# Optimization experiments

Measured on AMD Instinct MI355X. Metric: run time of the kernel, lower is better.

## Reference

```python
import jax, jax.numpy as jnp
import numpy as np

N_WIRES = 8
DIM = 2 ** N_WIRES  # 256 amplitudes
# PauliZ sign table: Z_SIGNS[w, i] = +1 if bit w of basis index i is 0 else -1
_bits = (np.arange(DIM)[None, :] >> (N_WIRES - 1 - np.arange(N_WIRES))[:, None]) & 1
Z_SIGNS = jnp.asarray(1.0 - 2.0 * _bits, dtype=jnp.float32)  # [8, 256]


def quantum_project(t, theta):
    """Batched 8-wire circuit: RX(x_w) encoder + trainable RX(theta_w) (RX gates on the
    same wire compose additively), then CNOT ring, then <Z_w> for each wire.
    t: [B, S, E] -> returns [B, S, H, 8]."""
    B, S, E = t.shape
    H = E // N_WIRES
    ang = (t.reshape(B, S, H, N_WIRES) + theta) * 0.5  # RX(a)RX(b)=RX(a+b)
    q0 = jnp.cos(ang).astype(jnp.complex64)
    q1 = (-1j * jnp.sin(ang)).astype(jnp.complex64)
    # Build product state |psi> = \otimes_w [cos(a_w/2), -i sin(a_w/2)] -> [B,S,H,256]
    state = jnp.ones((B, S, H, 1), jnp.complex64)
    for w in range(N_WIRES):
        qb = jnp.stack([q0[..., w], q1[..., w]], axis=-1)  # [B,S,H,2]
        state = (state[..., :, None] * qb[..., None, :]).reshape(B, S, H, -1)
    state = state.reshape((B, S, H) + (2,) * N_WIRES)  # wire w on axis 3+w
    # CNOT chain 0->1,...,6->7 then ring-closing 7->0
    for cw, tw in [(w, w + 1) for w in range(N_WIRES - 1)] + [(N_WIRES - 1, 0)]:
        s0 = jax.lax.index_in_dim(state, 0, axis=3 + cw, keepdims=True)
        s1 = jnp.flip(jax.lax.index_in_dim(state, 1, axis=3 + cw, keepdims=True), axis=3 + tw)
        state = jnp.concatenate([s0, s1], axis=3 + cw)
    amps = state.reshape(B, S, H, DIM)
    probs = amps.real * amps.real + amps.imag * amps.imag  # [B,S,H,256] float32
    return jnp.einsum('bshd,wd->bshw', probs, Z_SIGNS)  # <Z_w> per wire


def setup_inputs() -> dict:
    key = jax.random.key(0)
    kx, kq, kk, kv, ko, kt = jax.random.split(key, 6)
    B, S, E = 16, 512, 64
    scale = 1.0 / np.sqrt(E)
    return {
        'x': jax.random.normal(kx, (B, S, E), dtype=jnp.float32),
        'Wq': jax.random.normal(kq, (E, E), dtype=jnp.float32) * scale,
        'Wk': jax.random.normal(kk, (E, E), dtype=jnp.float32) * scale,
        'Wv': jax.random.normal(kv, (E, E), dtype=jnp.float32) * scale,
        'Wo': jax.random.normal(ko, (E, E), dtype=jnp.float32) * scale,
        'theta': jax.random.uniform(kt, (N_WIRES,), dtype=jnp.float32, minval=0.0, maxval=2.0 * np.pi),
    }


def reference(x, Wq, Wk, Wv, Wo, theta):
    B, S, E = x.shape
    q = quantum_project(x @ Wq.T, theta)  # [B,S,H,8]
    k = quantum_project(x @ Wk.T, theta)
    v = quantum_project(x @ Wv.T, theta)
    # NOTE: original code never transposes heads to dim 1, so attention mixes HEADS
    # per token: scores [B,S,H,H]. Faithfully reproduced. d_k = 8.
    scores = jnp.einsum('bsiw,bsjw->bsij', q, k) / jnp.float32(np.sqrt(N_WIRES))
    attn = jax.nn.softmax(scores, axis=-1)  # dropout is identity in eval
    out = jnp.einsum('bsij,bsjw->bsiw', attn, v)  # [B,S,H,8]
    # original: out.transpose(1,2).contiguous().view(B,-1,E) -> scrambled layout
    out = out.transpose(0, 2, 1, 3).reshape(B, -1, E)
    return out @ Wo.T
```

## Files before the change

kernel.cpp:

```cpp
#include <hip/hip_runtime.h>


typedef float  f32x4  __attribute__((ext_vector_type(4)));
typedef short  bf16x8 __attribute__((ext_vector_type(8)));
typedef unsigned short u16;
typedef unsigned int   u32;

#define WRS 72
#define SPS 68

#define DPP_SHR_STEP(d, j, sh)                                                 \
    {                                                                          \
        float _t = __int_as_float(__builtin_amdgcn_update_dpp(                 \
            0x3f800000, __float_as_int(d), 0x110 + sh, 0xf, 0xf, false));      \
        d *= ((j) >= (sh)) ? _t : 1.0f;                                        \
    }

__device__ __forceinline__ void bfsplit2(float f0, float f1, u32& hh, u32& ll) {
    const u32 u0 = __float_as_uint(f0), u1 = __float_as_uint(f1);
    const u32 h0 = (u0 + 0x8000u) & 0xffff0000u;
    const u32 h1 = (u1 + 0x8000u) & 0xffff0000u;
    const float r0 = f0 - __uint_as_float(h0);
    const float r1 = f1 - __uint_as_float(h1);
    hh = __builtin_amdgcn_perm(h1, h0, 0x07060302u);
    ll = __builtin_amdgcn_perm(__float_as_uint(r1), __float_as_uint(r0),
                               0x07060302u);
}

__device__ __forceinline__ void cvt8(const float4 v0, const float4 v1,
                                     bf16x8& hi, bf16x8& lo) {
    union { bf16x8 v; u32 u[4]; } H, L;
    bfsplit2(v0.x, v0.y, H.u[0], L.u[0]);
    bfsplit2(v0.z, v0.w, H.u[1], L.u[1]);
    bfsplit2(v1.x, v1.y, H.u[2], L.u[2]);
    bfsplit2(v1.z, v1.w, H.u[3], L.u[3]);
    hi = H.v; lo = L.v;
}

#define MFMA3(acc, ah, al, bh, bl)                                             \
    acc = __builtin_amdgcn_mfma_f32_16x16x32_bf16(al, bh, acc, 0, 0, 0);       \
    acc = __builtin_amdgcn_mfma_f32_16x16x32_bf16(ah, bl, acc, 0, 0, 0);       \
    acc = __builtin_amdgcn_mfma_f32_16x16x32_bf16(ah, bh, acc, 0, 0, 0);

__global__ __launch_bounds__(256, 2)
void qattn_fused(const float* __restrict__ xg,
                 const float* __restrict__ wqg, const float* __restrict__ wkg,
                 const float* __restrict__ wvg, const float* __restrict__ wog,
                 const float* __restrict__ thg,
                 float* __restrict__ outg)
{
    __shared__ __align__(16) float sP[48 * SPS];
    __shared__ __align__(16) u16 sSh[16 * WRS];
    __shared__ __align__(16) u16 sSl[16 * WRS];

    const int tid  = threadIdx.x;
    const int lane = tid & 63;
    const int wg   = tid >> 6;
    const int l15  = lane & 15;
    const int quad = lane >> 4;
    const int j    = lane & 7;
    const int b    = blockIdx.x >> 5;
    const int g16  = blockIdx.x & 31;

    const float* xr = xg + ((size_t)(b * 512 + g16 * 16 + l15) * 64) + quad * 8;
    bf16x8 ah0, al0, ah1, al1;
    cvt8(*(const float4*)xr, *(const float4*)(xr + 4), ah0, al0);
    cvt8(*(const float4*)(xr + 32), *(const float4*)(xr + 36), ah1, al1);
    const float thf = thg[j];

    #pragma unroll
    for (int ia = 0; ia < 3; ++ia) {
        const int aid = wg * 3 + ia;
        const int m = aid >> 2, nt = aid & 3;
        const float* wm = (m == 0) ? wqg : ((m == 1) ? wkg : wvg);
        const float* wr = wm + (nt * 16 + l15) * 64 + quad * 8;
        bf16x8 bh0, bl0, bh1, bl1;
        cvt8(*(const float4*)wr, *(const float4*)(wr + 4), bh0, bl0);
        cvt8(*(const float4*)(wr + 32), *(const float4*)(wr + 36), bh1, bl1);
        f32x4 acc = {0.f, 0.f, 0.f, 0.f};
        MFMA3(acc, ah0, al0, bh0, bl0)
        MFMA3(acc, ah1, al1, bh1, bl1)
        #pragma unroll
        for (int r = 0; r < 4; ++r) {
            const float c = __cosf(acc[r] + thf);
            float d = c;
            DPP_SHR_STEP(d, j, 1)
            DPP_SHR_STEP(d, j, 2)
            DPP_SHR_STEP(d, j, 4)
            float ex = (j == 0) ? 1.0f : c;
            DPP_SHR_STEP(ex, j, 1)
            DPP_SHR_STEP(ex, j, 2)
            DPP_SHR_STEP(ex, j, 4)
            const int base = (m * 16 + quad * 4 + r) * SPS + nt * 16 + l15;
            if (j > 0)  sP[base]     = d;
            if (j == 7) sP[base - 7] = ex;
        }
    }

    const float* wor = wog + (wg * 16 + l15) * 64 + quad * 8;
    bf16x8 obh0, obl0, obh1, obl1;
    cvt8(*(const float4*)wor, *(const float4*)(wor + 4), obh0, obl0);
    cvt8(*(const float4*)(wor + 32), *(const float4*)(wor + 36), obh1, obl1);

    __syncthreads();

    if (wg < 2) {
        const int tg = wg * 8 + (lane >> 3);
        const int i  = j;
        const int qb = tg * SPS;
        const int kb = (16 + tg) * SPS;
        const int vb = (32 + tg) * SPS;
        float q[8];
        *(float4*)&q[0] = *(const float4*)&sP[qb + 8 * i];
        *(float4*)&q[4] = *(const float4*)&sP[qb + 8 * i + 4];
        float pr[8];
        float sum = 0.f;
        #pragma unroll
        for (int jj = 0; jj < 8; ++jj) {
            const float4 k0 = *(const float4*)&sP[kb + 8 * jj];
            const float4 k1 = *(const float4*)&sP[kb + 8 * jj + 4];
            float s = q[0] * k0.x;
            s = fmaf(q[1], k0.y, s); s = fmaf(q[2], k0.z, s);
            s = fmaf(q[3], k0.w, s); s = fmaf(q[4], k1.x, s);
            s = fmaf(q[5], k1.y, s); s = fmaf(q[6], k1.z, s);
            s = fmaf(q[7], k1.w, s);
            pr[jj] = __expf(s * 0.35355339059327373f);
            sum += pr[jj];
        }
        const float rinv = 1.0f / sum;
        float o[8];
        #pragma unroll
        for (int w = 0; w < 8; ++w) o[w] = 0.f;
        #pragma unroll
        for (int jj = 0; jj < 8; ++jj) {
            const float4 v0 = *(const float4*)&sP[vb + 8 * jj];
            const float4 v1 = *(const float4*)&sP[vb + 8 * jj + 4];
            const float a = pr[jj] * rinv;
            o[0] = fmaf(a, v0.x, o[0]); o[1] = fmaf(a, v0.y, o[1]);
            o[2] = fmaf(a, v0.z, o[2]); o[3] = fmaf(a, v0.w, o[3]);
            o[4] = fmaf(a, v1.x, o[4]); o[5] = fmaf(a, v1.y, o[5]);
            o[6] = fmaf(a, v1.z, o[6]); o[7] = fmaf(a, v1.w, o[7]);
        }
        u32 hh[4], ll[4];
        #pragma unroll
        for (int c = 0; c < 4; ++c)
            bfsplit2(o[2 * c], o[2 * c + 1], hh[c], ll[c]);
        const int so = (i * 2 + (tg >> 3)) * WRS + 8 * (tg & 7);
        *(uint4*)&sSh[so] = make_uint4(hh[0], hh[1], hh[2], hh[3]);
        *(uint4*)&sSl[so] = make_uint4(ll[0], ll[1], ll[2], ll[3]);
    }
    __syncthreads();

    {
        const int arow = l15 * WRS + quad * 8;
        const bf16x8 sh0 = *(const bf16x8*)&sSh[arow];
        const bf16x8 sh1 = *(const bf16x8*)&sSh[arow + 32];
        const bf16x8 sl0 = *(const bf16x8*)&sSl[arow];
        const bf16x8 sl1 = *(const bf16x8*)&sSl[arow + 32];
        f32x4 acc = {0.f, 0.f, 0.f, 0.f};
        MFMA3(acc, sh0, sl0, obh0, obl0)
        MFMA3(acc, sh1, sl1, obh1, obl1)
        const int e = wg * 16 + l15;
        #pragma unroll
        for (int r = 0; r < 4; ++r) {
            const int rho = quad * 4 + r;
            const int R   = (rho >> 1) * 64 + g16 * 2 + (rho & 1);
            outg[((size_t)(b * 512 + R)) * 64 + e] = acc[r];
        }
    }
}

extern "C" void kernel_launch(void* const* d_in, const int* in_sizes, int n_in,
                              void* d_out, int out_size, void* d_ws, size_t ws_size,
                              hipStream_t stream) {
    const float* x  = (const float*)d_in[0];
    const float* wq = (const float*)d_in[1];
    const float* wk = (const float*)d_in[2];
    const float* wv = (const float*)d_in[3];
    const float* wo = (const float*)d_in[4];
    const float* th = (const float*)d_in[5];
    float* out = (float*)d_out;
    qattn_fused<<<dim3(512), dim3(256), 0, stream>>>(x, wq, wk, wv, wo, th, out);
}
```

Baseline: 70.00 us.

## Precompute bf16 split weight fragments and use single-wave blocks of eight tokens

Adds a small pre-kernel that converts all four weight matrices into hi/lo bf16 MFMA fragments once, stored in workspace. The main kernel then becomes a single 64-thread wave per eight-token group over 1024 blocks, loading those fragments directly instead of converting weights per block. This removes redundant per-block fp32-to-bf16 conversion and the cross-wave split. In exchange it adds a second launch, and half of each MFMA is wasted because only eight of sixteen rows are valid. Each wave also does all twelve projection tiles serially.

```diff
diff --git a/kernel.cpp b/kernel.cpp
--- a/kernel.cpp
+++ b/kernel.cpp
@@ -42,41 +42,53 @@
     acc = __builtin_amdgcn_mfma_f32_16x16x32_bf16(ah, bl, acc, 0, 0, 0);       \
     acc = __builtin_amdgcn_mfma_f32_16x16x32_bf16(ah, bh, acc, 0, 0, 0);
 
-__global__ __launch_bounds__(256, 2)
-void qattn_fused(const float* __restrict__ xg,
-                 const float* __restrict__ wqg, const float* __restrict__ wkg,
-                 const float* __restrict__ wvg, const float* __restrict__ wog,
-                 const float* __restrict__ thg,
-                 float* __restrict__ outg)
+__global__ __launch_bounds__(256)
+void prep_w(const float* __restrict__ wqg, const float* __restrict__ wkg,
+            const float* __restrict__ wvg, const float* __restrict__ wog,
+            uint4* __restrict__ ws)
 {
-    __shared__ __align__(16) float sP[48 * SPS];
-    __shared__ __align__(16) u16 sSh[16 * WRS];
-    __shared__ __align__(16) u16 sSl[16 * WRS];
-
-    const int tid  = threadIdx.x;
-    const int lane = tid & 63;
-    const int wg   = tid >> 6;
+    const int t    = blockIdx.x * 256 + threadIdx.x;
+    const int frag = t >> 6, lane = t & 63;
+    const int m = frag >> 3, nt = (frag >> 1) & 3, kh = frag & 1;
+    const float* gm[4] = {wqg, wkg, wvg, wog};
+    const float* src = gm[m] + (nt * 16 + (lane & 15)) * 64
+                             + kh * 32 + (lane >> 4) * 8;
+    bf16x8 hi, lo;
+    cvt8(*(const float4*)src, *(const float4*)(src + 4), hi, lo);
+    ws[frag * 64 + lane]        = *(const uint4*)&hi;
+    ws[frag * 64 + lane + 2048] = *(const uint4*)&lo;
+}
+
+__global__ __launch_bounds__(64)
+void qattn_fused(const float* __restrict__ xg, const uint4* __restrict__ wf,
+                 const float* __restrict__ thg, float* __restrict__ outg)
+{
+    __shared__ __align__(16) float sP[24 * SPS];
+    __shared__ __align__(16) u16 sSh[8 * WRS];
+    __shared__ __align__(16) u16 sSl[8 * WRS];
+
+    const int lane = threadIdx.x;
     const int l15  = lane & 15;
     const int quad = lane >> 4;
     const int j    = lane & 7;
-    const int b    = blockIdx.x >> 5;
-    const int g16  = blockIdx.x & 31;
-
-    const float* xr = xg + ((size_t)(b * 512 + g16 * 16 + l15) * 64) + quad * 8;
+    const int b    = blockIdx.x >> 6;
+    const int oct  = blockIdx.x & 63;
+
+    const float* xr = xg + ((size_t)(b * 512 + oct * 8 + (l15 & 7)) * 64)
+                    + quad * 8;
     bf16x8 ah0, al0, ah1, al1;
     cvt8(*(const float4*)xr, *(const float4*)(xr + 4), ah0, al0);
     cvt8(*(const float4*)(xr + 32), *(const float4*)(xr + 36), ah1, al1);
     const float thf = thg[j];
 
     #pragma unroll
-    for (int ia = 0; ia < 3; ++ia) {
-        const int aid = wg * 3 + ia;
-        const int m = aid >> 2, nt = aid & 3;
-        const float* wm = (m == 0) ? wqg : ((m == 1) ? wkg : wvg);
-        const float* wr = wm + (nt * 16 + l15) * 64 + quad * 8;
-        bf16x8 bh0, bl0, bh1, bl1;
-        cvt8(*(const float4*)wr, *(const float4*)(wr + 4), bh0, bl0);
-        cvt8(*(const float4*)(wr + 32), *(const float4*)(wr + 36), bh1, bl1);
+    for (int job = 0; job < 12; ++job) {
+        const int m = job >> 2, nt = job & 3;
+        const int fid = job * 2;
+        const bf16x8 bh0 = *(const bf16x8*)&wf[fid * 64 + lane];
+        const bf16x8 bl0 = *(const bf16x8*)&wf[fid * 64 + lane + 2048];
+        const bf16x8 bh1 = *(const bf16x8*)&wf[(fid + 1) * 64 + lane];
+        const bf16x8 bl1 = *(const bf16x8*)&wf[(fid + 1) * 64 + lane + 2048];
         f32x4 acc = {0.f, 0.f, 0.f, 0.f};
         MFMA3(acc, ah0, al0, bh0, bl0)
         MFMA3(acc, ah1, al1, bh1, bl1)
@@ -91,25 +103,21 @@
             DPP_SHR_STEP(ex, j, 1)
             DPP_SHR_STEP(ex, j, 2)
             DPP_SHR_STEP(ex, j, 4)
-            const int base = (m * 16 + quad * 4 + r) * SPS + nt * 16 + l15;
-            if (j > 0)  sP[base]     = d;
-            if (j == 7) sP[base - 7] = ex;
-        }
-    }
-
-    const float* wor = wog + (wg * 16 + l15) * 64 + quad * 8;
-    bf16x8 obh0, obl0, obh1, obl1;
-    cvt8(*(const float4*)wor, *(const float4*)(wor + 4), obh0, obl0);
-    cvt8(*(const float4*)(wor + 32), *(const float4*)(wor + 36), obh1, obl1);
-
+            if (quad < 2) {
+                const int base = (m * 8 + quad * 4 + r) * SPS + nt * 16 + l15;
+                if (j > 0)  sP[base]     = d;
+                if (j == 7) sP[base - 7] = ex;
+            }
+        }
+    }
     __syncthreads();
 
-    if (wg < 2) {
-        const int tg = wg * 8 + (lane >> 3);
+    {
+        const int t  = lane >> 3;
         const int i  = j;
-        const int qb = tg * SPS;
-        const int kb = (16 + tg) * SPS;
-        const int vb = (32 + tg) * SPS;
+        const int qb = t * SPS;
+        const int kb = (8 + t) * SPS;
+        const int vb = (16 + t) * SPS;
         float q[8];
         *(float4*)&q[0] = *(const float4*)&sP[qb + 8 * i];
         *(float4*)&q[4] = *(const float4*)&sP[qb + 8 * i + 4];
@@ -145,27 +153,34 @@
         #pragma unroll
         for (int c = 0; c < 4; ++c)
             bfsplit2(o[2 * c], o[2 * c + 1], hh[c], ll[c]);
-        const int so = (i * 2 + (tg >> 3)) * WRS + 8 * (tg & 7);
+        const int so = i * WRS + t * 8;
         *(uint4*)&sSh[so] = make_uint4(hh[0], hh[1], hh[2], hh[3]);
         *(uint4*)&sSl[so] = make_uint4(ll[0], ll[1], ll[2], ll[3]);
     }
     __syncthreads();
 
-    {
-        const int arow = l15 * WRS + quad * 8;
-        const bf16x8 sh0 = *(const bf16x8*)&sSh[arow];
-        const bf16x8 sh1 = *(const bf16x8*)&sSh[arow + 32];
-        const bf16x8 sl0 = *(const bf16x8*)&sSl[arow];
-        const bf16x8 sl1 = *(const bf16x8*)&sSl[arow + 32];
+    const int arow = (l15 & 7) * WRS + quad * 8;
+    const bf16x8 sh0 = *(const bf16x8*)&sSh[arow];
+    const bf16x8 sh1 = *(const bf16x8*)&sSh[arow + 32];
+    const bf16x8 sl0 = *(const bf16x8*)&sSl[arow];
+    const bf16x8 sl1 = *(const bf16x8*)&sSl[arow + 32];
+    #pragma unroll
+    for (int nt = 0; nt < 4; ++nt) {
+        const int fid = (12 + nt) * 2;
+        const bf16x8 obh0 = *(const bf16x8*)&wf[fid * 64 + lane];
+        const bf16x8 obl0 = *(const bf16x8*)&wf[fid * 64 + lane + 2048];
+        const bf16x8 obh1 = *(const bf16x8*)&wf[(fid + 1) * 64 + lane];
+        const bf16x8 obl1 = *(const bf16x8*)&wf[(fid + 1) * 64 + lane + 2048];
         f32x4 acc = {0.f, 0.f, 0.f, 0.f};
         MFMA3(acc, sh0, sl0, obh0, obl0)
         MFMA3(acc, sh1, sl1, obh1, obl1)
-        const int e = wg * 16 + l15;
+        const int e = nt * 16 + l15;
         #pragma unroll
         for (int r = 0; r < 4; ++r) {
-            const int rho = quad * 4 + r;
-            const int R   = (rho >> 1) * 64 + g16 * 2 + (rho & 1);
-            outg[((size_t)(b * 512 + R)) * 64 + e] = acc[r];
+            if (quad < 2) {
+                const int R = (quad * 4 + r) * 64 + oct;
+                outg[((size_t)(b * 512 + R)) * 64 + e] = acc[r];
+            }
         }
     }
 }
@@ -180,5 +195,7 @@
     const float* wo = (const float*)d_in[4];
     const float* th = (const float*)d_in[5];
     float* out = (float*)d_out;
-    qattn_fused<<<dim3(512), dim3(256), 0, stream>>>(x, wq, wk, wv, wo, th, out);
-}
+    uint4* wf = (uint4*)d_ws;
+    prep_w<<<dim3(8), dim3(256), 0, stream>>>(wq, wk, wv, wo, wf);
+    qattn_fused<<<dim3(1024), dim3(64), 0, stream>>>(x, wf, th, out);
+}
```

Measured after the change: 81.53 us. 16.5% more time.

## Process 32 tokens per 512-thread block and prefetch Wo before projection

Applied to the files above, without the earlier changes.

Doubles the work per block: each block now handles 32 tokens with 8 waves (two token tiles), halving the grid to 256 blocks. The Wo weight load is issued early as raw floats and converted after the barrier, to overlap its latency with the projection phase. Output stores now cover 4 consecutive rows per 64-row stride, giving wider write runs. The cost is fewer blocks for the GPU's compute units, larger shared memory per block, and more waves idle during the attention phase.

```diff
diff --git a/kernel.cpp b/kernel.cpp
--- a/kernel.cpp
+++ b/kernel.cpp
@@ -42,16 +42,16 @@
     acc = __builtin_amdgcn_mfma_f32_16x16x32_bf16(ah, bl, acc, 0, 0, 0);       \
     acc = __builtin_amdgcn_mfma_f32_16x16x32_bf16(ah, bh, acc, 0, 0, 0);
 
-__global__ __launch_bounds__(256, 2)
+__global__ __launch_bounds__(512, 1)
 void qattn_fused(const float* __restrict__ xg,
                  const float* __restrict__ wqg, const float* __restrict__ wkg,
                  const float* __restrict__ wvg, const float* __restrict__ wog,
                  const float* __restrict__ thg,
                  float* __restrict__ outg)
 {
-    __shared__ __align__(16) float sP[48 * SPS];
-    __shared__ __align__(16) u16 sSh[16 * WRS];
-    __shared__ __align__(16) u16 sSl[16 * WRS];
+    __shared__ __align__(16) float sP[96 * SPS];
+    __shared__ __align__(16) u16 sSh[32 * WRS];
+    __shared__ __align__(16) u16 sSl[32 * WRS];
 
     const int tid  = threadIdx.x;
     const int lane = tid & 63;
@@ -59,19 +59,27 @@
     const int l15  = lane & 15;
     const int quad = lane >> 4;
     const int j    = lane & 7;
-    const int b    = blockIdx.x >> 5;
-    const int g16  = blockIdx.x & 31;
+    const int b    = blockIdx.x >> 4;
+    const int grp  = blockIdx.x & 15;
 
-    const float* xr = xg + ((size_t)(b * 512 + g16 * 16 + l15) * 64) + quad * 8;
+    const int mt = wg & 1;
+    const float* xr = xg + ((size_t)(b * 512 + grp * 32 + mt * 16 + l15) * 64)
+                    + quad * 8;
     bf16x8 ah0, al0, ah1, al1;
     cvt8(*(const float4*)xr, *(const float4*)(xr + 4), ah0, al0);
     cvt8(*(const float4*)(xr + 32), *(const float4*)(xr + 36), ah1, al1);
     const float thf = thg[j];
 
+    const float* wor = wog + ((wg & 3) * 16 + l15) * 64 + quad * 8;
+    const float4 wo0 = *(const float4*)wor;
+    const float4 wo1 = *(const float4*)(wor + 4);
+    const float4 wo2 = *(const float4*)(wor + 32);
+    const float4 wo3 = *(const float4*)(wor + 36);
+
     #pragma unroll
     for (int ia = 0; ia < 3; ++ia) {
-        const int aid = wg * 3 + ia;
-        const int m = aid >> 2, nt = aid & 3;
+        const int jid = (wg >> 1) * 3 + ia;
+        const int m = jid >> 2, nt = jid & 3;
         const float* wm = (m == 0) ? wqg : ((m == 1) ? wkg : wvg);
         const float* wr = wm + (nt * 16 + l15) * 64 + quad * 8;
         bf16x8 bh0, bl0, bh1, bl1;
@@ -91,25 +99,24 @@
             DPP_SHR_STEP(ex, j, 1)
             DPP_SHR_STEP(ex, j, 2)
             DPP_SHR_STEP(ex, j, 4)
-            const int base = (m * 16 + quad * 4 + r) * SPS + nt * 16 + l15;
+            const int row  = m * 32 + mt * 16 + quad * 4 + r;
+            const int base = row * SPS + nt * 16 + l15;
             if (j > 0)  sP[base]     = d;
             if (j == 7) sP[base - 7] = ex;
         }
     }
-
-    const float* wor = wog + (wg * 16 + l15) * 64 + quad * 8;
-    bf16x8 obh0, obl0, obh1, obl1;
-    cvt8(*(const float4*)wor, *(const float4*)(wor + 4), obh0, obl0);
-    cvt8(*(const float4*)(wor + 32), *(const float4*)(wor + 36), obh1, obl1);
-
     __syncthreads();
 
-    if (wg < 2) {
+    bf16x8 obh0, obl0, obh1, obl1;
+    cvt8(wo0, wo1, obh0, obl0);
+    cvt8(wo2, wo3, obh1, obl1);
+
+    if (wg < 4) {
         const int tg = wg * 8 + (lane >> 3);
         const int i  = j;
         const int qb = tg * SPS;
-        const int kb = (16 + tg) * SPS;
-        const int vb = (32 + tg) * SPS;
+        const int kb = (32 + tg) * SPS;
+        const int vb = (64 + tg) * SPS;
         float q[8];
         *(float4*)&q[0] = *(const float4*)&sP[qb + 8 * i];
         *(float4*)&q[4] = *(const float4*)&sP[qb + 8 * i + 4];
@@ -145,14 +152,15 @@
         #pragma unroll
         for (int c = 0; c < 4; ++c)
             bfsplit2(o[2 * c], o[2 * c + 1], hh[c], ll[c]);
-        const int so = (i * 2 + (tg >> 3)) * WRS + 8 * (tg & 7);
+        const int so = (i * 4 + (tg >> 3)) * WRS + 8 * (tg & 7);
         *(uint4*)&sSh[so] = make_uint4(hh[0], hh[1], hh[2], hh[3]);
         *(uint4*)&sSl[so] = make_uint4(ll[0], ll[1], ll[2], ll[3]);
     }
     __syncthreads();
 
     {
-        const int arow = l15 * WRS + quad * 8;
+        const int mt2 = wg >> 2, nt2 = wg & 3;
+        const int arow = (mt2 * 16 + l15) * WRS + quad * 8;
         const bf16x8 sh0 = *(const bf16x8*)&sSh[arow];
         const bf16x8 sh1 = *(const bf16x8*)&sSh[arow + 32];
         const bf16x8 sl0 = *(const bf16x8*)&sSl[arow];
@@ -160,11 +168,11 @@
         f32x4 acc = {0.f, 0.f, 0.f, 0.f};
         MFMA3(acc, sh0, sl0, obh0, obl0)
         MFMA3(acc, sh1, sl1, obh1, obl1)
-        const int e = wg * 16 + l15;
+        const int e = nt2 * 16 + l15;
         #pragma unroll
         for (int r = 0; r < 4; ++r) {
-            const int rho = quad * 4 + r;
-            const int R   = (rho >> 1) * 64 + g16 * 2 + (rho & 1);
+            const int rho = mt2 * 16 + quad * 4 + r;
+            const int R   = (rho >> 2) * 64 + grp * 4 + (rho & 3);
             outg[((size_t)(b * 512 + R)) * 64 + e] = acc[r];
         }
     }
@@ -180,5 +188,5 @@
     const float* wo = (const float*)d_in[4];
     const float* th = (const float*)d_in[5];
     float* out = (float*)d_out;
-    qattn_fused<<<dim3(512), dim3(256), 0, stream>>>(x, wq, wk, wv, wo, th, out);
+    qattn_fused<<<dim3(256), dim3(512), 0, stream>>>(x, wq, wk, wv, wo, th, out);
 }
```

Result: no change. 69.51 us (-0.7%).
